# Kernel tuning notes

Hardware: AMD Instinct MI355X
Metric: run time of the kernel (lower is better)

## Reference

```python
import jax, jax.numpy as jnp
import numpy as np

N_NODES = 50000
N_EDGES = 1600000
IN_DIM = 128
HID = 64
EPS = 1e-6


def setup_inputs() -> dict:
    key = jax.random.key(0)
    ks = jax.random.split(key, 12)
    def g(k, shape, scale):
        return jax.random.normal(k, shape, dtype=jnp.float32) * scale
    x = g(ks[0], (N_NODES, IN_DIM), 1.0)
    edge_index = jax.random.randint(ks[1], (2, N_EDGES), 0, N_NODES, dtype=jnp.int64)
    return {
        "x": x,
        "edge_index": edge_index,
        "w0s": g(ks[2], (IN_DIM, HID), 1.0 / np.sqrt(IN_DIM)),
        "w0n": g(ks[3], (IN_DIM, HID), 1.0 / np.sqrt(IN_DIM)),
        "w1s": g(ks[4], (HID, HID), 1.0 / np.sqrt(HID)),
        "w1n": g(ks[5], (HID, HID), 1.0 / np.sqrt(HID)),
        "w2s": g(ks[6], (HID, HID), 1.0 / np.sqrt(HID)),
        "w2n": g(ks[7], (HID, HID), 1.0 / np.sqrt(HID)),
        "mw1": g(ks[8], (HID, 32), 1.0 / np.sqrt(HID)),
        "mb1": jnp.zeros((32,), jnp.float32),
        "mw2": g(ks[9], (32, 1), 1.0 / np.sqrt(32.0)),
        "mb2": jnp.zeros((1,), jnp.float32),
    }


def _uhg_layer(h, src, dst, inv_deg, ws, wn):
    # transform-then-gather (cheaper: GEMM at node granularity, gather at edge granularity)
    msg = (h @ wn)[src]                                    # [E, HID]
    agg = jax.ops.segment_sum(msg, dst, num_segments=N_NODES) * inv_deg  # mean over in-neighbors
    h2 = jax.nn.relu(h @ ws + agg)
    # projective (UHG) normalization: map embedding back onto the unit sphere / projective rep
    return h2 / (jnp.linalg.norm(h2, axis=-1, keepdims=True) + EPS)


def reference(x, edge_index, w0s, w0n, w1s, w1n, w2s, w2n, mw1, mb1, mw2, mb2):
    src, dst = edge_index[0], edge_index[1]
    deg = jax.ops.segment_sum(jnp.ones((N_EDGES,), jnp.float32), dst, num_segments=N_NODES)
    inv_deg = (1.0 / jnp.maximum(deg, 1.0))[:, None]       # [N,1]
    h = _uhg_layer(x, src, dst, inv_deg, w0s, w0n)
    h = _uhg_layer(h, src, dst, inv_deg, w1s, w1n)
    h = _uhg_layer(h, src, dst, inv_deg, w2s, w2n)
    h = jax.nn.relu(h @ mw1 + mb1)                         # [N,32]
    return jax.nn.sigmoid(h @ mw2 + mb2)                   # [N,1]
```

## Files before the change

kernel.cpp:

```cpp
#include <hip/hip_runtime.h>
#include <hip/hip_bf16.h>
#include <math.h>

#define N_NODES 50000
#define N_EDGES 1600000
#define IN_DIM  128
#define HID     64
#define EPB     8192
#define NBLK    196
#define NB      391
#define CAP     8192
#define PBKT    8192
static constexpr float EPS = 1e-6f;

typedef __attribute__((ext_vector_type(8))) short          short8;
typedef __attribute__((ext_vector_type(4))) int            i32x4;
typedef __attribute__((ext_vector_type(4))) float          f32x4;
typedef __attribute__((ext_vector_type(2))) float          f32x2;

__device__ __forceinline__ unsigned short f2bf(float f) {
    union { float f; unsigned int i; } c; c.f = f;
    unsigned int r = c.i + 0x7FFFu + ((c.i >> 16) & 1u);
    return (unsigned short)(r >> 16);
}
__device__ __forceinline__ unsigned char f2fp8(float f) {
    int p = __builtin_amdgcn_cvt_pk_fp8_f32(f, f, 0, false);
    return (unsigned char)(p & 0xff);
}


template <int K>
__device__ __forceinline__ void pack_body(const float* __restrict__ wS,
                                          const float* __restrict__ wN,
                                          unsigned short* __restrict__ pS,
                                          unsigned short* __restrict__ pN, int blk) {
    constexpr int NSLOT = (K / 32) * 4 * 64;
    int slot = blk * 256 + (int)threadIdx.x;
    if (slot >= NSLOT) return;
    int lane = slot & 63;
    int ct   = slot >> 6;
    int t    = ct & 3;
    int c    = ct >> 2;
    int m    = lane & 15;
    int quad = lane >> 4;
    int col  = t * 16 + m;
#pragma unroll
    for (int j = 0; j < 8; ++j) {
        int k = c * 32 + quad * 8 + j;
        pS[slot * 8 + j] = f2bf(wS[k * 64 + col]);
        pN[slot * 8 + j] = f2bf(wN[k * 64 + col]);
    }
}


__global__ __launch_bounds__(256) void bucket_count_pack(
    const int* __restrict__ ei, int* __restrict__ blockCounts,
    const float* __restrict__ w0s, const float* __restrict__ w0n,
    const float* __restrict__ w1s, const float* __restrict__ w1n,
    const float* __restrict__ w2s, const float* __restrict__ w2n,
    unsigned short* __restrict__ p0S, unsigned short* __restrict__ p0N,
    unsigned short* __restrict__ p1S, unsigned short* __restrict__ p1N,
    unsigned short* __restrict__ p2S, unsigned short* __restrict__ p2N,
    unsigned char* __restrict__ hnqA, unsigned char* __restrict__ hnqB) {
    if (blockIdx.x >= NBLK) {
        int blk = blockIdx.x - NBLK;
        if (blk == 7) {
            if (threadIdx.x >= 128 && threadIdx.x < 144)
                ((unsigned int*)(hnqA + (size_t)N_NODES * HID))[threadIdx.x - 128] = 0u;
            if (threadIdx.x >= 144 && threadIdx.x < 160)
                ((unsigned int*)(hnqB + (size_t)N_NODES * HID))[threadIdx.x - 144] = 0u;
        }
        if (blk < 4)      pack_body<IN_DIM>(w0s, w0n, p0S, p0N, blk);
        else if (blk < 6) pack_body<HID>(w1s, w1n, p1S, p1N, blk - 4);
        else              pack_body<HID>(w2s, w2n, p2S, p2N, blk - 6);
        return;
    }
    __shared__ int hist[NB];
    for (int i = threadIdx.x; i < NB; i += 256) hist[i] = 0;
    __syncthreads();
    int base = blockIdx.x * EPB;
    int lim  = min(EPB, N_EDGES - base);
    for (int i = threadIdx.x; i < lim; i += 256)
        atomicAdd(&hist[ei[N_EDGES + base + i] >> 7], 1);
    __syncthreads();
    for (int b = threadIdx.x; b < NB; b += 256)
        blockCounts[blockIdx.x * NB + b] = hist[b];
}

template <int K, bool F32IN>
__device__ __forceinline__ void gemm_body(
    const void* __restrict__ Av,
    const unsigned short* __restrict__ pS,
    const unsigned short* __restrict__ pN,
    float* __restrict__ hs, unsigned char* __restrict__ hnq, int blk) {
    constexpr int NC = K / 32;
    int lane = threadIdx.x & 63;
    int wv   = threadIdx.x >> 6;
    int tile = blk * 4 + wv;
    if (tile >= N_NODES / 16) return;
    int m    = lane & 15;
    int quad = lane >> 4;

    const short8* pSf = (const short8*)pS;
    const short8* pNf = (const short8*)pN;

    f32x4 accS[4], accN[4];
#pragma unroll
    for (int t = 0; t < 4; ++t) {
        accS[t] = (f32x4){0.f, 0.f, 0.f, 0.f};
        accN[t] = (f32x4){0.f, 0.f, 0.f, 0.f};
    }
#pragma unroll
    for (int c = 0; c < NC; ++c) {
        short8 a;
        if constexpr (F32IN) {
            const float* Af = (const float*)Av + ((size_t)tile * 16 + m) * K + quad * 8 + c * 32;
            f32x4 a0 = *(const f32x4*)Af;
            f32x4 a1 = *(const f32x4*)(Af + 4);
#pragma unroll
            for (int k = 0; k < 4; ++k) a[k]     = (short)f2bf(a0[k]);
#pragma unroll
            for (int k = 0; k < 4; ++k) a[k + 4] = (short)f2bf(a1[k]);
        } else {
            const short8* Af = (const short8*)((const unsigned short*)Av +
                               ((size_t)tile * 16 + m) * K + quad * 8);
            a = Af[c * 4];
        }
#pragma unroll
        for (int t = 0; t < 4; ++t) {
            short8 bs = pSf[(c * 4 + t) * 64 + lane];
            short8 bn = pNf[(c * 4 + t) * 64 + lane];
            accS[t] = __builtin_amdgcn_mfma_f32_16x16x32_bf16(a, bs, accS[t], 0, 0, 0);
            accN[t] = __builtin_amdgcn_mfma_f32_16x16x32_bf16(a, bn, accN[t], 0, 0, 0);
        }
    }
    int row0 = tile * 16 + quad * 4;
#pragma unroll
    for (int t = 0; t < 4; ++t) {
#pragma unroll
        for (int r = 0; r < 4; ++r) {
            size_t o = (size_t)(row0 + r) * HID + t * 16 + m;
            hs[o]  = accS[t][r];
            hnq[o] = f2fp8(accN[t][r]);
        }
    }
}

__global__ __launch_bounds__(256) void col_sum_gemm0(
    const int* __restrict__ blockCounts, int* __restrict__ totals,
    const float* __restrict__ x,
    const unsigned short* __restrict__ p0S, const unsigned short* __restrict__ p0N,
    float* __restrict__ hs, unsigned char* __restrict__ hnq) {
    if (blockIdx.x >= NB) {
        gemm_body<IN_DIM, true>(x, p0S, p0N, hs, hnq, blockIdx.x - NB);
        return;
    }
    __shared__ int ws[4];
    int b = blockIdx.x;
    int s = 0;
    for (int i = threadIdx.x; i < NBLK; i += 256) s += blockCounts[i * NB + b];
#pragma unroll
    for (int off = 32; off >= 1; off >>= 1) s += __shfl_xor(s, off, 64);
    if ((threadIdx.x & 63) == 0) ws[threadIdx.x >> 6] = s;
    __syncthreads();
    if (threadIdx.x == 0) totals[b] = ws[0] + ws[1] + ws[2] + ws[3];
}

__global__ __launch_bounds__(256) void col_fix_base(int* __restrict__ blockCounts,
                                                    const int* __restrict__ totals,
                                                    int* __restrict__ bucketBase) {
    __shared__ int vals[NBLK];
    __shared__ int sbase;
    int b = blockIdx.x;
    for (int i = threadIdx.x; i < NBLK; i += 256) vals[i] = blockCounts[i * NB + b];
    if (threadIdx.x < 64) {
        int lane = threadIdx.x;
        int s = 0;
        for (int i = lane; i < b; i += 64) s += totals[i];
#pragma unroll
        for (int off = 32; off >= 1; off >>= 1) s += __shfl_xor(s, off, 64);
        if (lane == 0) {
            sbase = s;
            bucketBase[b] = s;
            if (b == NB - 1) bucketBase[NB] = s + totals[b];
        }
    }
    __syncthreads();
    if (threadIdx.x < 64) {
        int lane  = threadIdx.x;
        int carry = sbase;
        for (int base = 0; base < NBLK; base += 64) {
            int i = base + lane;
            int v = (i < NBLK) ? vals[i] : 0;
            int incl = v;
#pragma unroll
            for (int off = 1; off < 64; off <<= 1) {
                int t = __shfl_up(incl, off, 64);
                if (lane >= off) incl += t;
            }
            if (i < NBLK) vals[i] = carry + incl - v;
            carry += __shfl(incl, 63, 64);
        }
    }
    __syncthreads();
    for (int i = threadIdx.x; i < NBLK; i += 256) blockCounts[i * NB + b] = vals[i];
}

__global__ __launch_bounds__(256) void bucket_scatter(const int* __restrict__ ei,
                                                      const int* __restrict__ blockCounts,
                                                      unsigned int* __restrict__ bucketPacked) {
    __shared__ int cur[NB];
    for (int b = threadIdx.x; b < NB; b += 256)
        cur[b] = blockCounts[blockIdx.x * NB + b];
    __syncthreads();
    int base = blockIdx.x * EPB;
    int lim  = min(EPB, N_EDGES - base);
    for (int i = threadIdx.x; i < lim; i += 256) {
        int s = ei[base + i];
        int d = ei[N_EDGES + base + i];
        int pos = atomicAdd(&cur[d >> 7], 1);
        bucketPacked[pos] = ((unsigned int)s << 7) | (unsigned int)(d & 127);
    }
}

__global__ __launch_bounds__(256) void node_scan_scatter_pad(
    const unsigned int* __restrict__ bucketPacked, const int* __restrict__ bucketBase,
    int* __restrict__ pbeg, int* __restrict__ rdeg, int* __restrict__ csr_pad) {
    __shared__ int cnt[128];
    __shared__ int half0;
    __shared__ unsigned int stage[CAP];
    int tid = threadIdx.x;
    if (tid < 128) cnt[tid] = 0;
    __syncthreads();
    int beg = bucketBase[blockIdx.x], end = bucketBase[blockIdx.x + 1];
    int n = end - beg;
    for (int i = tid; i < n; i += 256) {
        unsigned int e = bucketPacked[beg + i];
        if (i < CAP) stage[i] = e;
        atomicAdd(&cnt[e & 127], 1);
    }
    __syncthreads();
    int lane = tid & 63;
    int v    = (tid < 128) ? cnt[tid] : 0;
    int vp   = (v + 7) & ~7;
    int incl = vp;
#pragma unroll
    for (int off = 1; off < 64; off <<= 1) {
        int t = __shfl_up(incl, off, 64);
        if (lane >= off) incl += t;
    }
    if (tid == 63) half0 = incl;
    __syncthreads();
    int start = blockIdx.x * PBKT + ((tid >= 64 && tid < 128) ? half0 : 0) + incl - vp;
    int node  = blockIdx.x * 128 + tid;
    if (tid < 128 && node < N_NODES) {
        pbeg[node] = start;
        rdeg[node] = v;
        for (int j = v; j < vp; ++j) csr_pad[start + j] = N_NODES;
        cnt[tid] = start;
    }
    __syncthreads();
    for (int i = tid; i < n; i += 256) {
        unsigned int e = (i < CAP) ? stage[i] : bucketPacked[beg + i];
        int pos = atomicAdd(&cnt[e & 127], 1);
        csr_pad[pos] = (int)(e >> 7);
    }
}

template <bool MLP>
__global__ __launch_bounds__(256) void agg_update(
    const int* __restrict__ pbeg, const int* __restrict__ rdeg,
    const int* __restrict__ csr_pad,
    const unsigned char* __restrict__ hnq, const float* __restrict__ hs,
    const unsigned short* __restrict__ pS, const unsigned short* __restrict__ pN,
    float* __restrict__ hs2, unsigned char* __restrict__ hnq2,
    const float* __restrict__ mw1, const float* __restrict__ mb1,
    const float* __restrict__ mw2, const float* __restrict__ mb2,
    float* __restrict__ out) {
    __shared__ unsigned short sA[MLP ? 1 : 16 * 80];
    __shared__ float sW1[MLP ? HID * 32 : 1];
    __shared__ float sW2[MLP ? 32 : 1];
    __shared__ float sB1[MLP ? 32 : 1];
    __shared__ float sH[MLP ? 16 * 68 : 1];
    if (MLP) {
        for (int i = threadIdx.x; i < HID * 32; i += 256) sW1[i] = mw1[i];
        if (threadIdx.x < 32) { sW2[threadIdx.x] = mw2[threadIdx.x]; sB1[threadIdx.x] = mb1[threadIdx.x]; }
        __syncthreads();
    }
    int sn   = threadIdx.x >> 4;
    int r    = threadIdx.x & 15;
    int node = blockIdx.x * 16 + sn;
    int beg  = pbeg[node];
    int dg   = rdeg[node];
    f32x4 h  = *(const f32x4*)(hs + (size_t)node * HID + r * 4);
    int nbat = (dg + 7) >> 3;
    const i32x4* ip = (const i32x4*)(csr_pad + beg);
    unsigned r4 = (unsigned)(r * 4);

    f32x2 acc2[2];
    acc2[0] = (f32x2){0.f, 0.f};
    acc2[1] = (f32x2){0.f, 0.f};

#pragma unroll 2
    for (int t = 0; t < nbat; ++t) {
        i32x4 a = ip[2 * t];
        i32x4 b = ip[2 * t + 1];
        unsigned wv[8];
#pragma unroll
        for (int u = 0; u < 4; ++u)
            wv[u]     = *(const unsigned*)(hnq + (((unsigned)a[u] << 6) + r4));
#pragma unroll
        for (int u = 0; u < 4; ++u)
            wv[u + 4] = *(const unsigned*)(hnq + (((unsigned)b[u] << 6) + r4));
#pragma unroll
        for (int u = 0; u < 8; ++u) {
#if __has_builtin(__builtin_amdgcn_cvt_pk_f32_fp8)
            acc2[0] += __builtin_amdgcn_cvt_pk_f32_fp8((int)wv[u], false);
            acc2[1] += __builtin_amdgcn_cvt_pk_f32_fp8((int)wv[u], true);
#else
            acc2[0] += (f32x2){__builtin_amdgcn_cvt_f32_fp8((int)wv[u], 0),
                               __builtin_amdgcn_cvt_f32_fp8((int)wv[u], 1)};
            acc2[1] += (f32x2){__builtin_amdgcn_cvt_f32_fp8((int)wv[u], 2),
                               __builtin_amdgcn_cvt_f32_fp8((int)wv[u], 3)};
#endif
        }
    }

    float acc[4] = {acc2[0][0], acc2[0][1], acc2[1][0], acc2[1][1]};
    float invdeg = 1.0f / fmaxf((float)dg, 1.0f);
    float v[4], ss = 0.f;
#pragma unroll
    for (int k = 0; k < 4; ++k) {
        v[k] = fmaxf(fmaf(acc[k], invdeg, h[k]), 0.f);
        ss += v[k] * v[k];
    }
    ss += __shfl_xor(ss, 1, 64);
    ss += __shfl_xor(ss, 2, 64);
    ss += __shfl_xor(ss, 4, 64);
    ss += __shfl_xor(ss, 8, 64);
    float rs = 1.0f / (sqrtf(ss) + EPS);

    if constexpr (!MLP) {
        unsigned short* ap = &sA[sn * 80 + r * 4];
#pragma unroll
        for (int k = 0; k < 4; ++k) ap[k] = f2bf(v[k] * rs);
        __syncthreads();
        int lane = threadIdx.x & 63;
        int wv_  = threadIdx.x >> 6;
        int m    = lane & 15;
        int quad = lane >> 4;
        const short8* pB = (const short8*)((wv_ < 2) ? pS : pN);
        int t0 = (wv_ & 1) * 2;
        f32x4 gacc[2];
        gacc[0] = (f32x4){0.f, 0.f, 0.f, 0.f};
        gacc[1] = (f32x4){0.f, 0.f, 0.f, 0.f};
#pragma unroll
        for (int c = 0; c < 2; ++c) {
            short8 a = *(const short8*)&sA[m * 80 + quad * 8 + c * 32];
#pragma unroll
            for (int tt = 0; tt < 2; ++tt) {
                short8 b = pB[(c * 4 + t0 + tt) * 64 + lane];
                gacc[tt] = __builtin_amdgcn_mfma_f32_16x16x32_bf16(a, b, gacc[tt], 0, 0, 0);
            }
        }
        int row0 = blockIdx.x * 16 + quad * 4;
#pragma unroll
        for (int tt = 0; tt < 2; ++tt) {
            int col = (t0 + tt) * 16 + m;
#pragma unroll
            for (int rr = 0; rr < 4; ++rr) {
                size_t o = (size_t)(row0 + rr) * HID + col;
                if (wv_ < 2) hs2[o]  = gacc[tt][rr];
                else         hnq2[o] = f2fp8(gacc[tt][rr]);
            }
        }
    } else {
#pragma unroll
        for (int k = 0; k < 4; ++k) sH[sn * 68 + r * 4 + k] = v[k] * rs;
        __syncthreads();
        int c0 = r * 2;
        float y0 = sB1[c0], y1 = sB1[c0 + 1];
        const float* hrow2 = &sH[sn * 68];
#pragma unroll 8
        for (int k = 0; k < HID; ++k) {
            float hv = hrow2[k];
            y0 = fmaf(hv, sW1[k * 32 + c0], y0);
            y1 = fmaf(hv, sW1[k * 32 + c0 + 1], y1);
        }
        float p = fmaxf(y0, 0.f) * sW2[c0] + fmaxf(y1, 0.f) * sW2[c0 + 1];
        p += __shfl_xor(p, 1, 64);
        p += __shfl_xor(p, 2, 64);
        p += __shfl_xor(p, 4, 64);
        p += __shfl_xor(p, 8, 64);
        if (r == 0) out[node] = 1.0f / (1.0f + __expf(-(p + mb2[0])));
    }
}

extern "C" void kernel_launch(void* const* d_in, const int* in_sizes, int n_in,
                              void* d_out, int out_size, void* d_ws, size_t ws_size,
                              hipStream_t stream) {
    const float* x   = (const float*)d_in[0];
    const int*   ei  = (const int*)d_in[1];
    const float* w0s = (const float*)d_in[2];
    const float* w0n = (const float*)d_in[3];
    const float* w1s = (const float*)d_in[4];
    const float* w1n = (const float*)d_in[5];
    const float* w2s = (const float*)d_in[6];
    const float* w2n = (const float*)d_in[7];
    const float* mw1 = (const float*)d_in[8];
    const float* mb1 = (const float*)d_in[9];
    const float* mw2 = (const float*)d_in[10];
    const float* mb2 = (const float*)d_in[11];
    float*       out = (float*)d_out;

    int* pbeg        = (int*)d_ws;
    int* rdeg        = pbeg + 50048;
    int* blockCounts = rdeg + 50048;
    int* bucketBase  = blockCounts + 76800;
    int* totals      = bucketBase + 512;
    unsigned int* bucketPacked = (unsigned int*)(totals + 512);
    int* csr_pad     = (int*)(bucketPacked + N_EDGES);
    const size_t NH = (size_t)N_NODES * HID;
    float*          hsA  = (float*)(csr_pad + NB * PBKT);
    unsigned char*  hnqA = (unsigned char*)(hsA + NH);
    float*          hsB  = (float*)(hnqA + NH + 64);
    unsigned char*  hnqB = (unsigned char*)(hsB + NH);
    unsigned short* p0S = (unsigned short*)(hnqB + NH + 64);
    unsigned short* p0N = p0S + IN_DIM * HID;
    unsigned short* p1S = p0N + IN_DIM * HID;
    unsigned short* p1N = p1S + HID * HID;
    unsigned short* p2S = p1N + HID * HID;
    unsigned short* p2N = p2S + HID * HID;

    const int nodeGrid = N_NODES / 16;
    const int gemmGrid = (N_NODES / 16 + 3) / 4;

    bucket_count_pack<<<NBLK + 8, 256, 0, stream>>>(
        ei, blockCounts, w0s, w0n, w1s, w1n, w2s, w2n,
        p0S, p0N, p1S, p1N, p2S, p2N, hnqA, hnqB);
    col_sum_gemm0<<<NB + gemmGrid, 256, 0, stream>>>(
        blockCounts, totals, x, p0S, p0N, hsA, hnqA);
    col_fix_base<<<NB, 256, 0, stream>>>(blockCounts, totals, bucketBase);
    bucket_scatter<<<NBLK, 256, 0, stream>>>(ei, blockCounts, bucketPacked);
    node_scan_scatter_pad<<<NB, 256, 0, stream>>>(bucketPacked, bucketBase,
                                                  pbeg, rdeg, csr_pad);

    agg_update<false><<<nodeGrid, 256, 0, stream>>>(
        pbeg, rdeg, csr_pad, hnqA, hsA, p1S, p1N, hsB, hnqB,
        nullptr, nullptr, nullptr, nullptr, nullptr);

    agg_update<false><<<nodeGrid, 256, 0, stream>>>(
        pbeg, rdeg, csr_pad, hnqB, hsB, p2S, p2N, hsA, hnqA,
        nullptr, nullptr, nullptr, nullptr, nullptr);

    agg_update<true><<<nodeGrid, 256, 0, stream>>>(
        pbeg, rdeg, csr_pad, hnqA, hsA, nullptr, nullptr, nullptr, nullptr,
        mw1, mb1, mw2, mb2, out);
}
```

Baseline: 213.2 us.

## Merge bucket column-sum and prefix kernels using atomic global base allocation

```diff
diff --git a/kernel.cpp b/kernel.cpp
--- a/kernel.cpp
+++ b/kernel.cpp
@@ -6,11 +6,12 @@
 #define N_EDGES 1600000
 #define IN_DIM  128
 #define HID     64
-#define EPB     8192
-#define NBLK    196
+#define EPB     4096
+#define NBLK    391
 #define NB      391
 #define CAP     8192
 #define PBKT    8192
+#define GEMM0G  782
 static constexpr float EPS = 1e-6f;
 
 typedef __attribute__((ext_vector_type(8))) short          short8;
@@ -52,41 +53,6 @@
     }
 }
 
-
-__global__ __launch_bounds__(256) void bucket_count_pack(
-    const int* __restrict__ ei, int* __restrict__ blockCounts,
-    const float* __restrict__ w0s, const float* __restrict__ w0n,
-    const float* __restrict__ w1s, const float* __restrict__ w1n,
-    const float* __restrict__ w2s, const float* __restrict__ w2n,
-    unsigned short* __restrict__ p0S, unsigned short* __restrict__ p0N,
-    unsigned short* __restrict__ p1S, unsigned short* __restrict__ p1N,
-    unsigned short* __restrict__ p2S, unsigned short* __restrict__ p2N,
-    unsigned char* __restrict__ hnqA, unsigned char* __restrict__ hnqB) {
-    if (blockIdx.x >= NBLK) {
-        int blk = blockIdx.x - NBLK;
-        if (blk == 7) {
-            if (threadIdx.x >= 128 && threadIdx.x < 144)
-                ((unsigned int*)(hnqA + (size_t)N_NODES * HID))[threadIdx.x - 128] = 0u;
-            if (threadIdx.x >= 144 && threadIdx.x < 160)
-                ((unsigned int*)(hnqB + (size_t)N_NODES * HID))[threadIdx.x - 144] = 0u;
-        }
-        if (blk < 4)      pack_body<IN_DIM>(w0s, w0n, p0S, p0N, blk);
-        else if (blk < 6) pack_body<HID>(w1s, w1n, p1S, p1N, blk - 4);
-        else              pack_body<HID>(w2s, w2n, p2S, p2N, blk - 6);
-        return;
-    }
-    __shared__ int hist[NB];
-    for (int i = threadIdx.x; i < NB; i += 256) hist[i] = 0;
-    __syncthreads();
-    int base = blockIdx.x * EPB;
-    int lim  = min(EPB, N_EDGES - base);
-    for (int i = threadIdx.x; i < lim; i += 256)
-        atomicAdd(&hist[ei[N_EDGES + base + i] >> 7], 1);
-    __syncthreads();
-    for (int b = threadIdx.x; b < NB; b += 256)
-        blockCounts[blockIdx.x * NB + b] = hist[b];
-}
-
 template <int K, bool F32IN>
 __device__ __forceinline__ void gemm_body(
     const void* __restrict__ Av,
@@ -146,8 +112,45 @@
     }
 }
 
-__global__ __launch_bounds__(256) void col_sum_gemm0(
-    const int* __restrict__ blockCounts, int* __restrict__ totals,
+__global__ __launch_bounds__(256) void bucket_count_pack(
+    const int* __restrict__ ei, int* __restrict__ bc,
+    const float* __restrict__ w0s, const float* __restrict__ w0n,
+    const float* __restrict__ w1s, const float* __restrict__ w1n,
+    const float* __restrict__ w2s, const float* __restrict__ w2n,
+    unsigned short* __restrict__ p0S, unsigned short* __restrict__ p0N,
+    unsigned short* __restrict__ p1S, unsigned short* __restrict__ p1N,
+    unsigned short* __restrict__ p2S, unsigned short* __restrict__ p2N,
+    unsigned char* __restrict__ hnqA, unsigned char* __restrict__ hnqB,
+    int* __restrict__ gcount) {
+    if (blockIdx.x >= NBLK) {
+        int blk = blockIdx.x - NBLK;
+        if (blk == 7) {
+            if (threadIdx.x >= 128 && threadIdx.x < 144)
+                ((unsigned int*)(hnqA + (size_t)N_NODES * HID))[threadIdx.x - 128] = 0u;
+            if (threadIdx.x >= 144 && threadIdx.x < 160)
+                ((unsigned int*)(hnqB + (size_t)N_NODES * HID))[threadIdx.x - 144] = 0u;
+            if (threadIdx.x == 160) gcount[0] = 0;
+        }
+        if (blk < 4)      pack_body<IN_DIM>(w0s, w0n, p0S, p0N, blk);
+        else if (blk < 6) pack_body<HID>(w1s, w1n, p1S, p1N, blk - 4);
+        else              pack_body<HID>(w2s, w2n, p2S, p2N, blk - 6);
+        return;
+    }
+    __shared__ int hist[NB];
+    for (int i = threadIdx.x; i < NB; i += 256) hist[i] = 0;
+    __syncthreads();
+    int base = blockIdx.x * EPB;
+    int lim  = min(EPB, N_EDGES - base);
+    for (int i = threadIdx.x; i < lim; i += 256)
+        atomicAdd(&hist[ei[N_EDGES + base + i] >> 7], 1);
+    __syncthreads();
+    for (int b = threadIdx.x; b < NB; b += 256)
+        bc[blockIdx.x * NB + b] = hist[b];
+}
+
+__global__ __launch_bounds__(256) void col_sumfix_gemm0(
+    int* __restrict__ bc, int* __restrict__ bucketBase, int* __restrict__ bucketTot,
+    int* __restrict__ gcount,
     const float* __restrict__ x,
     const unsigned short* __restrict__ p0S, const unsigned short* __restrict__ p0N,
     float* __restrict__ hs, unsigned char* __restrict__ hnq) {
@@ -155,42 +158,26 @@
         gemm_body<IN_DIM, true>(x, p0S, p0N, hs, hnq, blockIdx.x - NB);
         return;
     }
-    __shared__ int ws[4];
+    __shared__ int vals[NBLK];
     int b = blockIdx.x;
-    int s = 0;
-    for (int i = threadIdx.x; i < NBLK; i += 256) s += blockCounts[i * NB + b];
-#pragma unroll
-    for (int off = 32; off >= 1; off >>= 1) s += __shfl_xor(s, off, 64);
-    if ((threadIdx.x & 63) == 0) ws[threadIdx.x >> 6] = s;
-    __syncthreads();
-    if (threadIdx.x == 0) totals[b] = ws[0] + ws[1] + ws[2] + ws[3];
-}
-
-__global__ __launch_bounds__(256) void col_fix_base(int* __restrict__ blockCounts,
-                                                    const int* __restrict__ totals,
-                                                    int* __restrict__ bucketBase) {
-    __shared__ int vals[NBLK];
-    __shared__ int sbase;
-    int b = blockIdx.x;
-    for (int i = threadIdx.x; i < NBLK; i += 256) vals[i] = blockCounts[i * NB + b];
+    for (int i = threadIdx.x; i < NBLK; i += 256) vals[i] = bc[i * NB + b];
+    __syncthreads();
     if (threadIdx.x < 64) {
         int lane = threadIdx.x;
         int s = 0;
-        for (int i = lane; i < b; i += 64) s += totals[i];
+        for (int i = lane; i < NBLK; i += 64) s += vals[i];
 #pragma unroll
         for (int off = 32; off >= 1; off >>= 1) s += __shfl_xor(s, off, 64);
+        int base = 0;
         if (lane == 0) {
-            sbase = s;
-            bucketBase[b] = s;
-            if (b == NB - 1) bucketBase[NB] = s + totals[b];
-        }
-    }
-    __syncthreads();
-    if (threadIdx.x < 64) {
-        int lane  = threadIdx.x;
-        int carry = sbase;
-        for (int base = 0; base < NBLK; base += 64) {
-            int i = base + lane;
+            base = atomicAdd(gcount, s);
+            bucketBase[b] = base;
+            bucketTot[b]  = s;
+        }
+        base = __shfl(base, 0, 64);
+        int carry = base;
+        for (int bs = 0; bs < NBLK; bs += 64) {
+            int i = bs + lane;
             int v = (i < NBLK) ? vals[i] : 0;
             int incl = v;
 #pragma unroll
@@ -203,15 +190,15 @@
         }
     }
     __syncthreads();
-    for (int i = threadIdx.x; i < NBLK; i += 256) blockCounts[i * NB + b] = vals[i];
+    for (int i = threadIdx.x; i < NBLK; i += 256) bc[i * NB + b] = vals[i];
 }
 
 __global__ __launch_bounds__(256) void bucket_scatter(const int* __restrict__ ei,
-                                                      const int* __restrict__ blockCounts,
+                                                      const int* __restrict__ bc,
                                                       unsigned int* __restrict__ bucketPacked) {
     __shared__ int cur[NB];
     for (int b = threadIdx.x; b < NB; b += 256)
-        cur[b] = blockCounts[blockIdx.x * NB + b];
+        cur[b] = bc[blockIdx.x * NB + b];
     __syncthreads();
     int base = blockIdx.x * EPB;
     int lim  = min(EPB, N_EDGES - base);
@@ -224,7 +211,8 @@
 }
 
 __global__ __launch_bounds__(256) void node_scan_scatter_pad(
-    const unsigned int* __restrict__ bucketPacked, const int* __restrict__ bucketBase,
+    const unsigned int* __restrict__ bucketPacked,
+    const int* __restrict__ bucketBase, const int* __restrict__ bucketTot,
     int* __restrict__ pbeg, int* __restrict__ rdeg, int* __restrict__ csr_pad) {
     __shared__ int cnt[128];
     __shared__ int half0;
@@ -232,8 +220,8 @@
     int tid = threadIdx.x;
     if (tid < 128) cnt[tid] = 0;
     __syncthreads();
-    int beg = bucketBase[blockIdx.x], end = bucketBase[blockIdx.x + 1];
-    int n = end - beg;
+    int beg = bucketBase[blockIdx.x];
+    int n   = bucketTot[blockIdx.x];
     for (int i = tid; i < n; i += 256) {
         unsigned int e = bucketPacked[beg + i];
         if (i < CAP) stage[i] = e;
@@ -415,10 +403,11 @@
 
     int* pbeg        = (int*)d_ws;
     int* rdeg        = pbeg + 50048;
-    int* blockCounts = rdeg + 50048;
-    int* bucketBase  = blockCounts + 76800;
-    int* totals      = bucketBase + 512;
-    unsigned int* bucketPacked = (unsigned int*)(totals + 512);
+    int* bc          = rdeg + 50048;
+    int* bucketBase  = bc + 153600;
+    int* bucketTot   = bucketBase + 512;
+    int* gcount      = bucketTot + 512;
+    unsigned int* bucketPacked = (unsigned int*)(gcount + 64);
     int* csr_pad     = (int*)(bucketPacked + N_EDGES);
     const size_t NH = (size_t)N_NODES * HID;
     float*          hsA  = (float*)(csr_pad + NB * PBKT);
@@ -433,16 +422,14 @@
     unsigned short* p2N = p2S + HID * HID;
 
     const int nodeGrid = N_NODES / 16;
-    const int gemmGrid = (N_NODES / 16 + 3) / 4;
 
     bucket_count_pack<<<NBLK + 8, 256, 0, stream>>>(
-        ei, blockCounts, w0s, w0n, w1s, w1n, w2s, w2n,
-        p0S, p0N, p1S, p1N, p2S, p2N, hnqA, hnqB);
-    col_sum_gemm0<<<NB + gemmGrid, 256, 0, stream>>>(
-        blockCounts, totals, x, p0S, p0N, hsA, hnqA);
-    col_fix_base<<<NB, 256, 0, stream>>>(blockCounts, totals, bucketBase);
-    bucket_scatter<<<NBLK, 256, 0, stream>>>(ei, blockCounts, bucketPacked);
-    node_scan_scatter_pad<<<NB, 256, 0, stream>>>(bucketPacked, bucketBase,
+        ei, bc, w0s, w0n, w1s, w1n, w2s, w2n,
+        p0S, p0N, p1S, p1N, p2S, p2N, hnqA, hnqB, gcount);
+    col_sumfix_gemm0<<<NB + GEMM0G, 256, 0, stream>>>(
+        bc, bucketBase, bucketTot, gcount, x, p0S, p0N, hsA, hnqA);
+    bucket_scatter<<<NBLK, 256, 0, stream>>>(ei, bc, bucketPacked);
+    node_scan_scatter_pad<<<NB, 256, 0, stream>>>(bucketPacked, bucketBase, bucketTot,
                                                   pbeg, rdeg, csr_pad);
 
     agg_update<false><<<nodeGrid, 256, 0, stream>>>(
```

Result: faster. 205.9 us (-3.4%).
